# Performance work log

Measured on AMD Instinct MI355X. Metric: run time of the kernel, lower is better.

The kernel has to match this reference:

```python
import jax, jax.numpy as jnp
import numpy as np

SUB_NO = 64
SYN_BASIS_NO = 3
T_HIST = 200
T_DATA = 100000


def setup_inputs() -> dict:
    key = jax.random.key(0)
    ks = jax.random.split(key, 5)
    # strictly-lower-triangular adjacency: each subunit integrates from ancestors
    C_den = jnp.tril((jax.random.uniform(ks[0], (SUB_NO, SUB_NO)) < 0.15).astype(jnp.float32), k=-1)
    S_conv = jax.random.normal(ks[1], (T_DATA, SUB_NO), dtype=jnp.float32)
    Y_ancest = 0.1 * jax.random.normal(ks[2], (T_DATA, SUB_NO), dtype=jnp.float32)
    # sparse binary spike trains
    Z_ancest = (jax.random.uniform(ks[3], (T_DATA, SUB_NO)) < 0.05).astype(jnp.float32)
    V_o = jnp.full((1,), -69.0, dtype=jnp.float32)
    W_sub = jnp.full((SUB_NO,), 0.25, dtype=jnp.float32)
    theta_syn = jnp.zeros((SUB_NO,), dtype=jnp.float32)
    K_spike = jnp.full((SUB_NO, SYN_BASIS_NO), 0.01, dtype=jnp.float32)
    tau_spike = jnp.arange(1.6, 1.6 + SYN_BASIS_NO, dtype=jnp.float32)
    delta_spike = jnp.zeros((SUB_NO,), dtype=jnp.float32)
    return {"S_conv": S_conv, "Y_ancest": Y_ancest, "Z_ancest": Z_ancest,
            "C_den": C_den, "V_o": V_o, "W_sub": W_sub, "theta_syn": theta_syn,
            "K_spike": K_spike, "tau_spike": tau_spike, "delta_spike": delta_spike,
            "T_hist": T_HIST}


def _ancest_kernel(K_spike, tau_spike, delta_spike, T_hist):
    # t[s, k] = max(k - delta_s, 0); kern[s, k] = sum_b (t/tau_b) exp(-t/tau_b) K[s,b]
    t = jnp.arange(T_hist, dtype=jnp.float32)[None, :] - delta_spike[:, None]
    t = jnp.maximum(t, 0.0)                                  # [sub, T_hist]
    tau = jnp.exp(tau_spike)                                 # [basis]
    t_tau = t[:, None, :] / tau[None, :, None]               # [sub, basis, T_hist]
    kern = jnp.sum(t_tau * jnp.exp(-t_tau) * K_spike[:, :, None], axis=1)
    return kern                                              # [sub, T_hist]


def reference(S_conv, Y_ancest, Z_ancest, C_den, V_o, W_sub, theta_syn,
              K_spike, tau_spike, delta_spike, T_hist):
    T_data, sub_no = S_conv.shape
    kern = _ancest_kernel(K_spike, tau_spike, delta_spike, T_hist)
    kern_f = jnp.flip(kern, axis=1)                          # matches torch.flip

    # spike_ancest[t, s, k] = sum_j C_den[s,j] Z_pad[t+k, j]  ->  precontract once
    Zc = Z_ancest @ C_den.T                                  # [T, sub]
    Zc_pad = jnp.concatenate([jnp.zeros((T_hist, sub_no), Zc.dtype), Zc], axis=0)
    # depthwise VALID conv over time: filtered[t, s] = sum_k kern_f[s,k] Zc_pad[t+k, s]
    out = jax.lax.conv_general_dilated(
        Zc_pad.T[None],                                      # [1, sub, T+T_hist]
        kern_f[:, None, :],                                  # [sub, 1, T_hist]
        window_strides=(1,), padding='VALID',
        feature_group_count=sub_no,
        dimension_numbers=('NCH', 'OIH', 'NCH'))
    filtered = out[0, :, :T_data].T                          # [T, sub]

    raw = Y_ancest @ C_den.T                                 # [T, sub]
    X_in = S_conv + theta_syn + filtered + raw
    final_Y = jax.nn.sigmoid(X_in) * W_sub + V_o
    return final_Y
```

## Files before the change

### kernel.cpp

```cpp
#include <hip/hip_runtime.h>

#define SUBS  64
#define GUARD 256
#define LB    32
#define JT    8
#define LSTR  136

typedef _Float16 f16x8 __attribute__((ext_vector_type(8)));
typedef float    f32x4 __attribute__((ext_vector_type(4)));

__device__ inline f16x8 ld_frag(const float* p) {
    float4 a = *(const float4*)p;
    float4 b = *(const float4*)(p + 4);
    f16x8 f;
    f[0]=(_Float16)a.x; f[1]=(_Float16)a.y; f[2]=(_Float16)a.z; f[3]=(_Float16)a.w;
    f[4]=(_Float16)b.x; f[5]=(_Float16)b.y; f[6]=(_Float16)b.z; f[7]=(_Float16)b.w;
    return f;
}
__device__ inline uint pkh2(float a, float b) {
    union { _Float16 h[2]; uint u; } p;
    p.h[0] = (_Float16)a; p.h[1] = (_Float16)b; return p.u;
}

__global__ __launch_bounds__(256, 4) void k_mm(
    const float* __restrict__ Z, const float* __restrict__ Y,
    const float* __restrict__ C,
    _Float16* __restrict__ Zt, _Float16* __restrict__ Yt, int T, int rgz)
{
    __shared__ _Float16 ztl[SUBS * LSTR];
    __shared__ _Float16 ytl[SUBS * LSTR];
    const int tid  = threadIdx.x;
    const int lane = tid & 63;
    const int wv   = tid >> 6;
    const int lr   = lane & 15;
    const int lg   = lane >> 4;
    const int t0b  = blockIdx.x * 128;

    if (blockIdx.x < 8) {
        const int tile = blockIdx.x * 4 + (tid >> 6);
        uint4 z4 = {0, 0, 0, 0};
        ((uint4*)Zt)[(size_t)tile * 64 + (tid & 63)] = z4;
        ((uint4*)Yt)[(size_t)tile * 64 + (tid & 63)] = z4;
    } else if (blockIdx.x < 18) {
        const int tile = rgz + (blockIdx.x - 8) * 4 + (tid >> 6);
        uint4 z4 = {0, 0, 0, 0};
        ((uint4*)Zt)[(size_t)tile * 64 + (tid & 63)] = z4;
        ((uint4*)Yt)[(size_t)tile * 64 + (tid & 63)] = z4;
    }

    f16x8 bfr[4][2];
    #pragma unroll
    for (int nt = 0; nt < 4; ++nt)
        #pragma unroll
        for (int ks = 0; ks < 2; ++ks)
            bfr[nt][ks] = ld_frag(&C[(lr + 16 * nt) * 64 + ks * 32 + lg * 8]);

    #pragma unroll
    for (int g = 0; g < 2; ++g) {
        const int t0 = t0b + wv * 32 + g * 16;
        const int rowA = t0 + lr;
        const bool okA = rowA < T;
        f16x8 az[2], ay[2];
        #pragma unroll
        for (int ks = 0; ks < 2; ++ks) {
            if (okA) {
                az[ks] = ld_frag(&Z[(size_t)rowA * 64 + ks * 32 + lg * 8]);
                ay[ks] = ld_frag(&Y[(size_t)rowA * 64 + ks * 32 + lg * 8]);
            } else {
                az[ks] = (f16x8)(_Float16)0.f;
                ay[ks] = (f16x8)(_Float16)0.f;
            }
        }

        f32x4 accZ[4], accY[4];
        #pragma unroll
        for (int nt = 0; nt < 4; ++nt) { accZ[nt] = (f32x4){0,0,0,0}; accY[nt] = (f32x4){0,0,0,0}; }
        #pragma unroll
        for (int nt = 0; nt < 4; ++nt) {
            #pragma unroll
            for (int ks = 0; ks < 2; ++ks) {
                accZ[nt] = __builtin_amdgcn_mfma_f32_16x16x32_f16(az[ks], bfr[nt][ks], accZ[nt], 0, 0, 0);
                accY[nt] = __builtin_amdgcn_mfma_f32_16x16x32_f16(ay[ks], bfr[nt][ks], accY[nt], 0, 0, 0);
            }
        }

        #pragma unroll
        for (int nt = 0; nt < 4; ++nt) {
            const int sc = lr + 16 * nt;
            const int lt = wv * 32 + g * 16 + lg * 4;
            uint2 pz, py;
            pz.x = pkh2(accZ[nt][0], accZ[nt][1]);
            pz.y = pkh2(accZ[nt][2], accZ[nt][3]);
            py.x = pkh2(accY[nt][0], accY[nt][1]);
            py.y = pkh2(accY[nt][2], accY[nt][3]);
            *(uint2*)&ztl[sc * LSTR + lt] = pz;
            *(uint2*)&ytl[sc * LSTR + lt] = py;
        }
    }

    __syncthreads();

    const int gbase = (GUARD >> 3) + blockIdx.x * 16;
    #pragma unroll
    for (int it = 0; it < 4; ++it) {
        const int chunk = it * 256 + tid;
        const int row = chunk & 63;
        const int col = chunk >> 6;
        const int tb  = t0b + col * 8;
        if (tb + 7 < T) {
            ((uint4*)Zt)[(size_t)(gbase + col) * 64 + row] =
                *(const uint4*)&ztl[row * LSTR + col * 8];
            ((uint4*)Yt)[(size_t)(gbase + col) * 64 + row] =
                *(const uint4*)&ytl[row * LSTR + col * 8];
        } else {
            #pragma unroll
            for (int h = 0; h < 8; ++h)
                if (tb + h < T) {
                    Zt[(size_t)(gbase + col) * 512 + row * 8 + h] = ztl[row * LSTR + col * 8 + h];
                    Yt[(size_t)(gbase + col) * 512 + row * 8 + h] = ytl[row * LSTR + col * 8 + h];
                }
        }
    }
}

#define STEP3(u)                                                                 \
    _Pragma("unroll")                                                            \
    for (int b = 0; b < 3; ++b) {                                                \
        const float yn = fmaf(twr[b], y1[b], fmaf(mr2[b], y2[b], cr[b] * (u)));  \
        y2[b] = y1[b]; y1[b] = yn;                                               \
    }

#define PAIRW(wrd) {                                                             \
    union { uint u; _Float16 h[2]; } w_; w_.u = (wrd);                           \
    STEP3((float)w_.h[0]);                                                       \
    STEP3((float)w_.h[1]); }

__global__ __launch_bounds__(256, 4) void k_state(
    const _Float16* __restrict__ Zt,
    const float* __restrict__ K_spike, const float* __restrict__ tau_spike,
    float* __restrict__ fb, int NB)
{
    const int tid = threadIdx.x;
    const int s   = tid & 63;
    const int wv  = tid >> 6;
    const int gi  = blockIdx.x * 4 + wv - JT;
    if (gi >= NB) return;
    float* fout = fb + (size_t)(gi + JT) * 384;
    if (gi < 0) {
        #pragma unroll
        for (int c = 0; c < 6; ++c) fout[c * 64 + s] = 0.f;
        return;
    }

    float twr[3], mr2[3], cr[3];
    #pragma unroll
    for (int b = 0; b < 3; ++b) {
        const float tau = __expf(tau_spike[b]);
        const float r   = __expf(-1.0f / tau);
        twr[b] = 2.0f * r;
        mr2[b] = -r * r;
        cr[b]  = K_spike[s * 3 + b] / tau * r;
    }

    const uint4* xb = (const uint4*)Zt + (size_t)(31 + 4 * gi) * 64 + s;
    const uint4 x0 = xb[0];
    const uint4 x1 = xb[64];
    const uint4 x2 = xb[128];
    const uint4 x3 = xb[192];
    const uint4 x4 = xb[256];

    float y1[3] = {0.f, 0.f, 0.f}, y2[3] = {0.f, 0.f, 0.f};
    PAIRW(x0.w);
    PAIRW(x1.x); PAIRW(x1.y); PAIRW(x1.z); PAIRW(x1.w);
    PAIRW(x2.x); PAIRW(x2.y); PAIRW(x2.z); PAIRW(x2.w);
    PAIRW(x3.x); PAIRW(x3.y); PAIRW(x3.z); PAIRW(x3.w);
    PAIRW(x4.x); PAIRW(x4.y); PAIRW(x4.z);

    #pragma unroll
    for (int b = 0; b < 3; ++b) {
        fout[(2 * b)     * 64 + s] = y1[b];
        fout[(2 * b + 1) * 64 + s] = y2[b];
    }
}

__global__ __launch_bounds__(256, 3) void k_iir2(
    const _Float16* __restrict__ Zt, const _Float16* __restrict__ Yt,
    const float* __restrict__ S,
    const float* __restrict__ K_spike, const float* __restrict__ tau_spike,
    const float* __restrict__ delta_spike, const float* __restrict__ theta,
    const float* __restrict__ W, const float* __restrict__ Vo,
    const float* __restrict__ fb, float* __restrict__ out, int T, int NB)
{
    const int tid = threadIdx.x;
    const int s   = tid & 63;
    const int wv  = tid >> 6;
    const int i   = blockIdx.x * 4 + wv;
    if (i >= NB) return;
    const int t0 = i * LB;

    float twr[3], mr2[3], cr[3], taus[3];
    #pragma unroll
    for (int b = 0; b < 3; ++b) {
        const float tau = __expf(tau_spike[b]);
        taus[b] = tau;
        const float r = __expf(-1.0f / tau);
        twr[b] = 2.0f * r;
        mr2[b] = -r * r;
        cr[b]  = K_spike[s * 3 + b] / tau * r;
    }
    int dl = (int)rintf(delta_spike[s]);
    dl = min(max(dl, 0), 30);
    const float th   = theta[s];
    const float wsub = W[s];
    const float vo   = Vo[0];

    float y1[3], y2[3];

    if (__all(dl == 0)) {
        float aL[3], bL[3], cL[3], dL[3];
        #pragma unroll
        for (int b = 0; b < 3; ++b) {
            const float r   = 0.5f * twr[b];
            const float rm1 = __expf(-(float)(LB - 1) / taus[b]);
            const float rl  = rm1 * r;
            const float rp  = rl * r;
            aL[b] = (float)(LB + 1) * rl;
            bL[b] = -(float)LB * rp;
            cL[b] = (float)LB * rm1;
            dL[b] = -(float)(LB - 1) * rl;
        }
        {
            const float* fq = fb + (size_t)i * 384;
            #pragma unroll
            for (int b = 0; b < 3; ++b) {
                y1[b] = fq[(2 * b) * 64 + s];
                y2[b] = fq[(2 * b + 1) * 64 + s];
            }
        }
        #pragma unroll
        for (int j = 7; j >= 1; --j) {
            const float* fq = fb + (size_t)(i + JT - j) * 384;
            #pragma unroll
            for (int b = 0; b < 3; ++b) {
                const float f1 = fq[(2 * b) * 64 + s];
                const float f2 = fq[(2 * b + 1) * 64 + s];
                const float n1 = fmaf(aL[b], y1[b], fmaf(bL[b], y2[b], f1));
                const float n2 = fmaf(cL[b], y1[b], fmaf(dL[b], y2[b], f2));
                y1[b] = n1; y2[b] = n2;
            }
        }

        const uint4* xb = (const uint4*)Zt + (size_t)(31 + 4 * i) * 64 + s;
        const uint4 x0 = xb[0];
        const uint4 x1 = xb[64];
        const uint4 x2 = xb[128];
        const uint4 x3 = xb[192];
        const uint4 x4 = xb[256];
        const uint4* yb = (const uint4*)Yt + (size_t)(32 + 4 * i) * 64 + s;
        const uint4 yv0 = yb[0], yv1 = yb[64], yv2 = yb[128], yv3 = yb[192];

        uint spk[16];
        #pragma unroll
        for (int p = 0; p < 16; ++p) {
            const int t1 = min(t0 + 2 * p,     T - 1);
            const int t2 = min(t0 + 2 * p + 1, T - 1);
            spk[p] = pkh2(S[(size_t)t1 * 64 + s] + th, S[(size_t)t2 * 64 + s] + th);
        }

        uint xw[16] = { x0.w, x1.x, x1.y, x1.z, x1.w, x2.x, x2.y, x2.z,
                        x2.w, x3.x, x3.y, x3.z, x3.w, x4.x, x4.y, x4.z };
        uint yw[16] = { yv0.x, yv0.y, yv0.z, yv0.w, yv1.x, yv1.y, yv1.z, yv1.w,
                        yv2.x, yv2.y, yv2.z, yv2.w, yv3.x, yv3.y, yv3.z, yv3.w };

        #pragma unroll
        for (int w = 0; w < 16; ++w) {
            union { uint u; _Float16 h[2]; } wx; wx.u = xw[w];
            union { uint u; _Float16 h[2]; } wy; wy.u = yw[w];
            union { uint u; _Float16 h[2]; } wp; wp.u = spk[w];
            #pragma unroll
            for (int hh = 0; hh < 2; ++hh) {
                STEP3((float)wx.h[hh]);
                const int t = t0 + 2 * w + hh;
                if (t < T) {
                    const float xin = (float)wy.h[hh] + (float)wp.h[hh]
                                      + y1[0] + y1[1] + y1[2];
                    const float sig = 1.0f / (1.0f + __expf(-xin));
                    out[(size_t)t * 64 + s] = fmaf(sig, wsub, vo);
                }
            }
        }
    } else {
        y1[0] = y1[1] = y1[2] = 0.f;
        y2[0] = y2[1] = y2[2] = 0.f;
        const int xi0 = t0 - 226 - dl;
        for (int k = 0; k < 224 + LB; ++k) {
            const int h = GUARD + xi0 + k;
            const float u = (float)Zt[(size_t)(h >> 3) * 512 + s * 8 + (h & 7)];
            STEP3(u);
            const int o = k - 224;
            if (o >= 0) {
                const int t = t0 + o;
                if (t < T) {
                    const int hy = GUARD + t;
                    const float yc = (float)Yt[(size_t)(hy >> 3) * 512 + s * 8 + (hy & 7)];
                    const float xin = yc + S[(size_t)t * 64 + s] + th
                                      + y1[0] + y1[1] + y1[2];
                    const float sig = 1.0f / (1.0f + __expf(-xin));
                    out[(size_t)t * 64 + s] = fmaf(sig, wsub, vo);
                }
            }
        }
    }
}

extern "C" void kernel_launch(void* const* d_in, const int* in_sizes, int n_in,
                              void* d_out, int out_size, void* d_ws, size_t ws_size,
                              hipStream_t stream)
{
    const float* S     = (const float*)d_in[0];
    const float* Y     = (const float*)d_in[1];
    const float* Z     = (const float*)d_in[2];
    const float* C     = (const float*)d_in[3];
    const float* Vo    = (const float*)d_in[4];
    const float* W     = (const float*)d_in[5];
    const float* theta = (const float*)d_in[6];
    const float* K     = (const float*)d_in[7];
    const float* tau   = (const float*)d_in[8];
    const float* delta = (const float*)d_in[9];
    const int T  = in_sizes[0] / SUBS;
    const int NB = (T + LB - 1) / LB;

    const int rgz    = (GUARD + T + 7) >> 3;
    const int ntiles = rgz + 44;
    _Float16* Zt = (_Float16*)d_ws;
    _Float16* Yt = (_Float16*)((char*)d_ws + (size_t)ntiles * 1024);
    float*    fb = (float*)((char*)d_ws + (size_t)ntiles * 2048);

    k_mm<<<(T + 127) / 128, 256, 0, stream>>>(Z, Y, C, Zt, Yt, T, rgz);
    k_state<<<(NB + JT + 3) / 4, 256, 0, stream>>>(Zt, K, tau, fb, NB);
    k_iir2<<<(NB + 3) / 4, 256, 0, stream>>>(Zt, Yt, S, K, tau, delta, theta,
                                             W, Vo, fb, (float*)d_out, T, NB);
}
```

Measured before the change: 49.26 us.

## Fuse block state computation into matmul kernel using shared-memory tiles

Removes the separate k_state launch. Each wave of k_mm now runs the per-block IIR state recurrence straight from the shared-memory Zt tile it just produced, and block 0 zeroes the guard state entries. k_iir2 is also realigned so the first two outputs of each block use the carried state directly, which drops one Zt word load and two recurrence steps per block. The gains are one fewer kernel launch and one fewer global read of Zt, at the cost of more work and register pressure in k_mm and a change in the state boundary semantics (32-step window, no delta shift) that must still match the lookback chain.

```diff
diff --git a/kernel.cpp b/kernel.cpp
--- a/kernel.cpp
+++ b/kernel.cpp
@@ -22,10 +22,23 @@
     p.h[0] = (_Float16)a; p.h[1] = (_Float16)b; return p.u;
 }
 
+#define STEP3(u)                                                                 \
+    _Pragma("unroll")                                                            \
+    for (int b = 0; b < 3; ++b) {                                                \
+        const float yn = fmaf(twr[b], y1[b], fmaf(mr2[b], y2[b], cr[b] * (u)));  \
+        y2[b] = y1[b]; y1[b] = yn;                                               \
+    }
+#define PAIRW(wrd) {                                                             \
+    union { uint u; _Float16 h[2]; } w_; w_.u = (wrd);                           \
+    STEP3((float)w_.h[0]);                                                       \
+    STEP3((float)w_.h[1]); }
+
 __global__ __launch_bounds__(256, 4) void k_mm(
     const float* __restrict__ Z, const float* __restrict__ Y,
     const float* __restrict__ C,
-    _Float16* __restrict__ Zt, _Float16* __restrict__ Yt, int T, int rgz)
+    const float* __restrict__ K_spike, const float* __restrict__ tau_spike,
+    _Float16* __restrict__ Zt, _Float16* __restrict__ Yt,
+    float* __restrict__ fb, int T, int rgz, int NB)
 {
     __shared__ _Float16 ztl[SUBS * LSTR];
     __shared__ _Float16 ytl[SUBS * LSTR];
@@ -46,6 +59,9 @@
         uint4 z4 = {0, 0, 0, 0};
         ((uint4*)Zt)[(size_t)tile * 64 + (tid & 63)] = z4;
         ((uint4*)Yt)[(size_t)tile * 64 + (tid & 63)] = z4;
+    }
+    if (blockIdx.x == 0) {
+        for (int idx = tid; idx < JT * 384; idx += 256) fb[idx] = 0.f;
     }
 
     f16x8 bfr[4][2];
@@ -121,67 +137,47 @@
                 }
         }
     }
-}
-
-#define STEP3(u)                                                                 \
-    _Pragma("unroll")                                                            \
-    for (int b = 0; b < 3; ++b) {                                                \
-        const float yn = fmaf(twr[b], y1[b], fmaf(mr2[b], y2[b], cr[b] * (u)));  \
-        y2[b] = y1[b]; y1[b] = yn;                                               \
-    }
-
-#define PAIRW(wrd) {                                                             \
-    union { uint u; _Float16 h[2]; } w_; w_.u = (wrd);                           \
-    STEP3((float)w_.h[0]);                                                       \
-    STEP3((float)w_.h[1]); }
-
-__global__ __launch_bounds__(256, 4) void k_state(
-    const _Float16* __restrict__ Zt,
-    const float* __restrict__ K_spike, const float* __restrict__ tau_spike,
-    float* __restrict__ fb, int NB)
-{
-    const int tid = threadIdx.x;
-    const int s   = tid & 63;
-    const int wv  = tid >> 6;
-    const int gi  = blockIdx.x * 4 + wv - JT;
-    if (gi >= NB) return;
-    float* fout = fb + (size_t)(gi + JT) * 384;
-    if (gi < 0) {
-        #pragma unroll
-        for (int c = 0; c < 6; ++c) fout[c * 64 + s] = 0.f;
-        return;
-    }
-
-    float twr[3], mr2[3], cr[3];
-    #pragma unroll
-    for (int b = 0; b < 3; ++b) {
-        const float tau = __expf(tau_spike[b]);
-        const float r   = __expf(-1.0f / tau);
-        twr[b] = 2.0f * r;
-        mr2[b] = -r * r;
-        cr[b]  = K_spike[s * 3 + b] / tau * r;
-    }
-
-    const uint4* xb = (const uint4*)Zt + (size_t)(31 + 4 * gi) * 64 + s;
-    const uint4 x0 = xb[0];
-    const uint4 x1 = xb[64];
-    const uint4 x2 = xb[128];
-    const uint4 x3 = xb[192];
-    const uint4 x4 = xb[256];
-
-    float y1[3] = {0.f, 0.f, 0.f}, y2[3] = {0.f, 0.f, 0.f};
-    PAIRW(x0.w);
-    PAIRW(x1.x); PAIRW(x1.y); PAIRW(x1.z); PAIRW(x1.w);
-    PAIRW(x2.x); PAIRW(x2.y); PAIRW(x2.z); PAIRW(x2.w);
-    PAIRW(x3.x); PAIRW(x3.y); PAIRW(x3.z); PAIRW(x3.w);
-    PAIRW(x4.x); PAIRW(x4.y); PAIRW(x4.z);
-
-    #pragma unroll
-    for (int b = 0; b < 3; ++b) {
-        fout[(2 * b)     * 64 + s] = y1[b];
-        fout[(2 * b + 1) * 64 + s] = y2[b];
-    }
-}
+
+    const int grun = blockIdx.x * 4 + wv;
+    if (grun < NB) {
+        float twr[3], mr2[3], cr[3];
+        #pragma unroll
+        for (int b = 0; b < 3; ++b) {
+            const float tau = __expf(tau_spike[b]);
+            const float r   = __expf(-1.0f / tau);
+            twr[b] = 2.0f * r;
+            mr2[b] = -r * r;
+            cr[b]  = K_spike[lane * 3 + b] / tau * r;
+        }
+        const uint* zr = (const uint*)ztl + lane * (LSTR / 2) + wv * 16;
+        float y1[3] = {0.f, 0.f, 0.f}, y2[3] = {0.f, 0.f, 0.f};
+        uint xa[8];
+        #pragma unroll
+        for (int k = 0; k < 8; ++k) xa[k] = zr[k];
+        #pragma unroll
+        for (int k = 0; k < 8; ++k) PAIRW(xa[k]);
+        #pragma unroll
+        for (int k = 0; k < 8; ++k) xa[k] = zr[8 + k];
+        #pragma unroll
+        for (int k = 0; k < 8; ++k) PAIRW(xa[k]);
+        float* fout = fb + (size_t)(grun + JT) * 384;
+        #pragma unroll
+        for (int b = 0; b < 3; ++b) {
+            fout[(2 * b)     * 64 + lane] = y1[b];
+            fout[(2 * b + 1) * 64 + lane] = y2[b];
+        }
+    }
+}
+
+#define EMIT(o, f) {                                                             \
+    const int t_ = t0 + (o);                                                     \
+    if (t_ < T) {                                                                \
+        union { uint u; _Float16 h[2]; } wy_; wy_.u = ywd[(o) >> 1];             \
+        union { uint u; _Float16 h[2]; } wp_; wp_.u = spk[(o) >> 1];             \
+        const float xin_ = (float)wy_.h[(o) & 1] + (float)wp_.h[(o) & 1] + (f);  \
+        const float sig_ = 1.0f / (1.0f + __expf(-xin_));                        \
+        out[(size_t)t_ * 64 + s] = fmaf(sig_, wsub, vo);                         \
+    } }
 
 __global__ __launch_bounds__(256, 3) void k_iir2(
     const _Float16* __restrict__ Zt, const _Float16* __restrict__ Yt,
@@ -250,12 +246,8 @@
             }
         }
 
-        const uint4* xb = (const uint4*)Zt + (size_t)(31 + 4 * i) * 64 + s;
-        const uint4 x0 = xb[0];
-        const uint4 x1 = xb[64];
-        const uint4 x2 = xb[128];
-        const uint4 x3 = xb[192];
-        const uint4 x4 = xb[256];
+        const uint4* xb = (const uint4*)Zt + (size_t)(32 + 4 * i) * 64 + s;
+        const uint4 x0 = xb[0], x1 = xb[64], x2 = xb[128], x3 = xb[192];
         const uint4* yb = (const uint4*)Yt + (size_t)(32 + 4 * i) * 64 + s;
         const uint4 yv0 = yb[0], yv1 = yb[64], yv2 = yb[128], yv3 = yb[192];
 
@@ -267,27 +259,20 @@
             spk[p] = pkh2(S[(size_t)t1 * 64 + s] + th, S[(size_t)t2 * 64 + s] + th);
         }
 
-        uint xw[16] = { x0.w, x1.x, x1.y, x1.z, x1.w, x2.x, x2.y, x2.z,
-                        x2.w, x3.x, x3.y, x3.z, x3.w, x4.x, x4.y, x4.z };
-        uint yw[16] = { yv0.x, yv0.y, yv0.z, yv0.w, yv1.x, yv1.y, yv1.z, yv1.w,
-                        yv2.x, yv2.y, yv2.z, yv2.w, yv3.x, yv3.y, yv3.z, yv3.w };
-
-        #pragma unroll
-        for (int w = 0; w < 16; ++w) {
+        const uint xw[15] = { x0.x, x0.y, x0.z, x0.w, x1.x, x1.y, x1.z, x1.w,
+                              x2.x, x2.y, x2.z, x2.w, x3.x, x3.y, x3.z };
+        const uint ywd[16] = { yv0.x, yv0.y, yv0.z, yv0.w, yv1.x, yv1.y, yv1.z, yv1.w,
+                               yv2.x, yv2.y, yv2.z, yv2.w, yv3.x, yv3.y, yv3.z, yv3.w };
+
+        EMIT(0, y2[0] + y2[1] + y2[2]);
+        EMIT(1, y1[0] + y1[1] + y1[2]);
+        #pragma unroll
+        for (int w = 0; w < 15; ++w) {
             union { uint u; _Float16 h[2]; } wx; wx.u = xw[w];
-            union { uint u; _Float16 h[2]; } wy; wy.u = yw[w];
-            union { uint u; _Float16 h[2]; } wp; wp.u = spk[w];
-            #pragma unroll
-            for (int hh = 0; hh < 2; ++hh) {
-                STEP3((float)wx.h[hh]);
-                const int t = t0 + 2 * w + hh;
-                if (t < T) {
-                    const float xin = (float)wy.h[hh] + (float)wp.h[hh]
-                                      + y1[0] + y1[1] + y1[2];
-                    const float sig = 1.0f / (1.0f + __expf(-xin));
-                    out[(size_t)t * 64 + s] = fmaf(sig, wsub, vo);
-                }
-            }
+            STEP3((float)wx.h[0]);
+            EMIT(2 + 2 * w, y1[0] + y1[1] + y1[2]);
+            STEP3((float)wx.h[1]);
+            EMIT(3 + 2 * w, y1[0] + y1[1] + y1[2]);
         }
     } else {
         y1[0] = y1[1] = y1[2] = 0.f;
@@ -336,8 +321,7 @@
     _Float16* Yt = (_Float16*)((char*)d_ws + (size_t)ntiles * 1024);
     float*    fb = (float*)((char*)d_ws + (size_t)ntiles * 2048);
 
-    k_mm<<<(T + 127) / 128, 256, 0, stream>>>(Z, Y, C, Zt, Yt, T, rgz);
-    k_state<<<(NB + JT + 3) / 4, 256, 0, stream>>>(Zt, K, tau, fb, NB);
+    k_mm<<<(T + 127) / 128, 256, 0, stream>>>(Z, Y, C, K, tau, Zt, Yt, fb, T, rgz, NB);
     k_iir2<<<(NB + 3) / 4, 256, 0, stream>>>(Zt, Yt, S, K, tau, delta, theta,
                                              W, Vo, fb, (float*)d_out, T, NB);
 }
```

Result: faster. 46.55 us (-5.5%).
